# Kernel optimization log

Measured on AMD Instinct MI355X. Metric: run time of the kernel, lower is better.

## Reference

```python
import jax, jax.numpy as jnp
import numpy as np

N_NODES = 50000


def _gcn_layer(x, W, b, src, dst, n_nodes):
    # GCNConv: h = D^{-1/2} (A + I) D^{-1/2} (x W) + b, with src/dst already
    # including self-loops.
    h = x @ W  # [N, out]
    deg = jax.ops.segment_sum(jnp.ones(src.shape, x.dtype), dst,
                              num_segments=n_nodes)  # [N]
    dinv = jnp.where(deg > 0, jax.lax.rsqrt(jnp.maximum(deg, 1e-12)), 0.0)
    norm = dinv[src] * dinv[dst]  # [E+N]
    msg = h[src] * norm[:, None]  # gathered + weighted messages
    out = jax.ops.segment_sum(msg, dst, num_segments=n_nodes)  # scatter-add
    return out + b


def setup_inputs() -> dict:
    key = jax.random.key(0)
    k0, k1, k2, k3 = jax.random.split(key, 4)
    d_in, hidden, n_edges = 128, 128, 800000
    x = jax.random.normal(k0, (N_NODES, d_in), dtype=jnp.float32)
    edge_index = jax.random.randint(k1, (2, n_edges), 0, N_NODES, dtype=jnp.int64)
    W1 = jax.random.normal(k2, (d_in, hidden), dtype=jnp.float32) * (1.0 / np.sqrt(d_in))
    b1 = jnp.zeros((hidden,), jnp.float32)
    W2 = jax.random.normal(k3, (hidden, hidden), dtype=jnp.float32) * (1.0 / np.sqrt(hidden))
    b2 = jnp.zeros((hidden,), jnp.float32)
    return {"x": x, "edge_index": edge_index, "W1": W1, "b1": b1,
            "W2": W2, "b2": b2}


def reference(x, edge_index, W1, b1, W2, b2):
    n = x.shape[0]
    loop = jnp.arange(n, dtype=edge_index.dtype)
    src = jnp.concatenate([edge_index[0], loop])  # add self-loops
    dst = jnp.concatenate([edge_index[1], loop])
    h = _gcn_layer(x, W1, b1, src, dst, n)
    h = jax.nn.relu(h)
    # dropout p=0.5 is identity in eval mode (self.training == False)
    h = _gcn_layer(h, W2, b2, src, dst, n)
    return jax.nn.log_softmax(h, axis=1)
```

## Files before the change

kernel.cpp:

```cpp
#include <hip/hip_runtime.h>
#include <math.h>

#define D 128
#define CAP 6144
#define EPB 4096

typedef __attribute__((ext_vector_type(8))) short bf16x8;
typedef __attribute__((ext_vector_type(4))) float f32x4;

__device__ __forceinline__ float bf_lo(unsigned u) { return __uint_as_float(u << 16); }
__device__ __forceinline__ float bf_hi(unsigned u) { return __uint_as_float(u & 0xFFFF0000u); }
__device__ __forceinline__ unsigned pack_bf16(float a, float b) {
    unsigned ua = __float_as_uint(a), ub = __float_as_uint(b);
    ua = (ua + 0x7FFFu + ((ua >> 16) & 1u)) >> 16;
    ub = (ub + 0x7FFFu + ((ub >> 16) & 1u)) >> 16;
    return ua | (ub << 16);
}

__device__ __forceinline__ int edge_at(const void* eidx, int i64, long long pos) {
    return i64 ? (int)((const long long*)eidx)[pos] : ((const int*)eidx)[pos];
}


template <int AF32>
__device__ __forceinline__ void gemm_body(char* lds, int bid, const void* Ain,
                                          const float* __restrict__ Wf,
                                          const unsigned* __restrict__ metaIn,
                                          unsigned char* __restrict__ y8,
                                          float* __restrict__ scales, int n) {
    int tid = threadIdx.x;
    #pragma unroll
    for (int it = 0; it < 32; ++it) {
        int idx = tid + it * 256;
        int c = idx & 127, k2 = idx >> 7;
        *(unsigned*)&lds[c * 272 + k2 * 4] =
            pack_bf16(Wf[(k2 * 2) * D + c], Wf[(k2 * 2 + 1) * D + c]);
    }
    int w = tid >> 6, l = tid & 63;
    int row0 = bid * 128;
    int rowA0 = row0 + w * 16 + (l & 15);
    int rowA1 = rowA0 + 64;
    int rA0 = rowA0 < n ? rowA0 : 0;
    int rA1 = rowA1 < n ? rowA1 : 0;
    __syncthreads();

    f32x4 acc[2][8];
    #pragma unroll
    for (int r = 0; r < 2; ++r)
        #pragma unroll
        for (int f = 0; f < 8; ++f) acc[r][f] = (f32x4)0.f;

    #pragma unroll
    for (int s = 0; s < 4; ++s) {
        bf16x8 a0, a1;
        if (AF32) {
            const float* Af = (const float*)Ain;
            const float4* p0 = (const float4*)(Af + (size_t)rA0 * D + ((l >> 4) << 3) + s * 32);
            const float4* p1 = (const float4*)(Af + (size_t)rA1 * D + ((l >> 4) << 3) + s * 32);
            float4 f0 = p0[0], f1 = p0[1], f2 = p1[0], f3 = p1[1];
            uint4 v0, v1;
            v0.x = pack_bf16(f0.x, f0.y); v0.y = pack_bf16(f0.z, f0.w);
            v0.z = pack_bf16(f1.x, f1.y); v0.w = pack_bf16(f1.z, f1.w);
            v1.x = pack_bf16(f2.x, f2.y); v1.y = pack_bf16(f2.z, f2.w);
            v1.z = pack_bf16(f3.x, f3.y); v1.w = pack_bf16(f3.z, f3.w);
            a0 = *(bf16x8*)&v0;
            a1 = *(bf16x8*)&v1;
        } else {
            const char* Ab = (const char*)Ain;
            a0 = *(const bf16x8*)(Ab + (size_t)rA0 * 256 + ((l >> 4) << 4) + s * 64);
            a1 = *(const bf16x8*)(Ab + (size_t)rA1 * 256 + ((l >> 4) << 4) + s * 64);
        }
        int boff = ((l >> 4) << 4) + s * 64;
        #pragma unroll
        for (int f = 0; f < 8; ++f) {
            bf16x8 b = *(const bf16x8*)&lds[(f * 16 + (l & 15)) * 272 + boff];
            acc[0][f] = __builtin_amdgcn_mfma_f32_16x16x32_bf16(a0, b, acc[0][f], 0, 0, 0);
            acc[1][f] = __builtin_amdgcn_mfma_f32_16x16x32_bf16(a1, b, acc[1][f], 0, 0, 0);
        }
    }

    float* fl = (float*)lds;
    #pragma unroll
    for (int r = 0; r < 2; ++r) {
        __syncthreads();
        {
            int rbase = w * 16 + ((l >> 4) << 2);
            #pragma unroll
            for (int f = 0; f < 8; ++f) {
                int c = f * 16 + (l & 15);
                #pragma unroll
                for (int j = 0; j < 4; ++j)
                    fl[(rbase + j) * 132 + c] = acc[r][f][j];
            }
        }
        __syncthreads();
        int row = tid >> 2, cseg = (tid & 3) << 5;
        int gr = row0 + r * 64 + row;
        if (gr < n) {
            float z[32];
            #pragma unroll
            for (int i = 0; i < 32; ++i) z[i] = fl[row * 132 + cseg + i];
            float mx = 0.f;
            #pragma unroll
            for (int i = 0; i < 32; ++i) mx = fmaxf(mx, fabsf(z[i]));
            mx = fmaxf(mx, __shfl_xor(mx, 1));
            mx = fmaxf(mx, __shfl_xor(mx, 2));
            float inv = mx > 0.f ? 127.0f / mx : 0.f;
            unsigned q[8];
            #pragma unroll
            for (int j = 0; j < 8; ++j) {
                int q0 = __float2int_rn(z[j * 4 + 0] * inv);
                int q1 = __float2int_rn(z[j * 4 + 1] * inv);
                int q2 = __float2int_rn(z[j * 4 + 2] * inv);
                int q3 = __float2int_rn(z[j * 4 + 3] * inv);
                q[j] = (q0 & 255) | ((q1 & 255) << 8) | ((q2 & 255) << 16) | ((q3 & 255) << 24);
            }
            uint4* op = (uint4*)(y8 + (size_t)gr * 128 + cseg);
            op[0] = make_uint4(q[0], q[1], q[2], q[3]);
            op[1] = make_uint4(q[4], q[5], q[6], q[7]);
            if ((tid & 3) == 0) {
                float sc = mx * (1.0f / 127.0f);
                if (metaIn)
                    sc *= (float)(metaIn[gr] >> 17) * (1.0f / 32767.0f);
                scales[gr] = sc;
            }
        }
    }
}


__global__ void __launch_bounds__(256) k_prep(const void* eidx, int* bcnt,
                                              unsigned* __restrict__ binned, int e,
                                              const float* __restrict__ x,
                                              const float* __restrict__ W1,
                                              unsigned char* __restrict__ y8,
                                              float* __restrict__ scales,
                                              int n, int ebk) {
    __shared__ char lds[35840];
    int b = blockIdx.x, t = threadIdx.x;

    if (b >= ebk) {
        gemm_body<1>(lds, b - ebk, x, W1, nullptr, y8, scales, n);
        return;
    }

    int* hist = (int*)lds;
    int* gbase = hist + 256;
    int* lcur = gbase + 256;
    uint2* ed = (uint2*)(lds + 3072);

    const int* e32 = (const int*)eidx;
    int i64 = 1;
    #pragma unroll
    for (int j = 1; j < 32; j += 2)
        if (e32[j] != 0) i64 = 0;

    hist[t] = 0;
    lcur[t] = 0;
    __syncthreads();
    long long base = (long long)b * EPB;
    #pragma unroll
    for (int k = 0; k < EPB / 256; ++k) {
        long long i = base + k * 256 + t;
        if (i < e) {
            int s = edge_at(eidx, i64, i);
            int d = edge_at(eidx, i64, (long long)e + i);
            ed[k * 256 + t] = make_uint2((unsigned)s, (unsigned)d);
            atomicAdd(&hist[d >> 8], 1);
        }
    }
    __syncthreads();
    int c = hist[t];
    gbase[t] = c ? atomicAdd(&bcnt[t], c) : 0;
    __syncthreads();
    long long rem = e - base;
    int lim = (rem < EPB) ? (int)rem : EPB;
    for (int j = t; j < lim; j += 256) {
        uint2 sd = ed[j];
        int bk = sd.y >> 8;
        int off = gbase[bk] + atomicAdd(&lcur[bk], 1);
        if (off >= CAP) off = CAP - 1;
        binned[(size_t)bk * CAP + off] = sd.x | ((sd.y & 255u) << 17);
    }
}


__global__ void __launch_bounds__(256) k_binB(const unsigned* __restrict__ binned,
                                              const int* __restrict__ bcnt,
                                              const float* __restrict__ scales1,
                                              unsigned* __restrict__ meta,
                                              float* __restrict__ fs1,
                                              float* __restrict__ fs2,
                                              unsigned* __restrict__ csr64,
                                              int n) {
    __shared__ int lcur[256];
    int b = blockIdx.x, t = threadIdx.x;
    if (b == 0) {
        if (t == 0) meta[n] = 0;
        if (t == 1) fs1[n] = 0.f;
        if (t == 2) fs2[n] = 0.f;
    }
    lcur[t] = 0;
    __syncthreads();

    int cnt = bcnt[b];
    if (cnt > CAP) cnt = CAP;
    unsigned nodebase = (unsigned)b << 8;
    for (int i = t; i < cnt; i += 256) {
        unsigned en = binned[(size_t)b * CAP + i];
        unsigned src = en & 0x1FFFF;
        unsigned dl = en >> 17;
        int pos = atomicAdd(&lcur[dl], 1);
        if (pos < 64)
            csr64[(size_t)(nodebase + dl) * 64 + pos] = src;
    }
    __syncthreads();

    int node = b * 256 + t;
    if (node < n) {
        int dv = lcur[t];
        int filled = dv < 64 ? dv : 64;
        int pend = (filled + 7) & ~7;
        for (int j = filled; j < pend; ++j)
            csr64[(size_t)node * 64 + j] = (unsigned)n;
        unsigned q = __float2uint_rn(rsqrtf((float)(dv + 1)) * 32767.0f);
        meta[node] = (q << 17) | (unsigned)(pend >> 3);
        fs1[node] = ((float)q * (1.0f / 32767.0f)) * scales1[node];
    }
}


template <int EPI>
__global__ void __launch_bounds__(256) k_agg(const unsigned char* __restrict__ Y8,
                                             const float* __restrict__ fs,
                                             const unsigned* __restrict__ meta,
                                             const unsigned* __restrict__ csr64,
                                             const float* __restrict__ bias,
                                             void* __restrict__ outp, int n) {
    int node = __builtin_amdgcn_readfirstlane(blockIdx.x * 4 + (threadIdx.x >> 6));
    if (node >= n) return;
    int lane = threadIdx.x & 63;
    unsigned mt = meta[node];
    int pend = (mt & 15) << 3;
    float di = (float)(mt >> 17) * (1.0f / 32767.0f);
    const unsigned* cp = csr64 + (size_t)node * 64;
    const unsigned short* Yu = (const unsigned short*)Y8;

    unsigned su = Yu[(size_t)node * 64 + lane];
    float fself = fs[node];
    float ax = fself * (float)(char)(su & 255);
    float ay = fself * (float)(char)(su >> 8);

    for (int e = 0; e < pend; e += 8) {
        unsigned s0 = cp[e + 0], s1 = cp[e + 1], s2 = cp[e + 2], s3 = cp[e + 3];
        unsigned s4 = cp[e + 4], s5 = cp[e + 5], s6 = cp[e + 6], s7 = cp[e + 7];
        unsigned u0 = Yu[(size_t)s0 * 64 + lane];
        unsigned u1 = Yu[(size_t)s1 * 64 + lane];
        unsigned u2 = Yu[(size_t)s2 * 64 + lane];
        unsigned u3 = Yu[(size_t)s3 * 64 + lane];
        unsigned u4 = Yu[(size_t)s4 * 64 + lane];
        unsigned u5 = Yu[(size_t)s5 * 64 + lane];
        unsigned u6 = Yu[(size_t)s6 * 64 + lane];
        unsigned u7 = Yu[(size_t)s7 * 64 + lane];
        float f0 = fs[s0], f1 = fs[s1], f2 = fs[s2], f3 = fs[s3];
        float f4 = fs[s4], f5 = fs[s5], f6 = fs[s6], f7 = fs[s7];
        ax += f0 * (float)(char)(u0 & 255) + f1 * (float)(char)(u1 & 255)
            + f2 * (float)(char)(u2 & 255) + f3 * (float)(char)(u3 & 255)
            + f4 * (float)(char)(u4 & 255) + f5 * (float)(char)(u5 & 255)
            + f6 * (float)(char)(u6 & 255) + f7 * (float)(char)(u7 & 255);
        ay += f0 * (float)(char)(u0 >> 8) + f1 * (float)(char)(u1 >> 8)
            + f2 * (float)(char)(u2 >> 8) + f3 * (float)(char)(u3 >> 8)
            + f4 * (float)(char)(u4 >> 8) + f5 * (float)(char)(u5 >> 8)
            + f6 * (float)(char)(u6 >> 8) + f7 * (float)(char)(u7 >> 8);
    }

    float2 bv = ((const float2*)bias)[lane];
    float z0 = di * ax + bv.x;
    float z1 = di * ay + bv.y;

    if (EPI == 0) {
        ((unsigned*)outp)[(size_t)node * 64 + lane] =
            pack_bf16(fmaxf(z0, 0.f), fmaxf(z1, 0.f));
    } else {
        float m = fmaxf(z0, z1);
        #pragma unroll
        for (int off = 1; off < 64; off <<= 1) m = fmaxf(m, __shfl_xor(m, off));
        float s = __expf(z0 - m) + __expf(z1 - m);
        #pragma unroll
        for (int off = 1; off < 64; off <<= 1) s += __shfl_xor(s, off);
        float lse = m + __logf(s);
        ((float2*)outp)[(size_t)node * 64 + lane] = make_float2(z0 - lse, z1 - lse);
    }
}


__global__ void __launch_bounds__(256) k_gemm2(const unsigned* __restrict__ h,
                                               const float* __restrict__ W2,
                                               const unsigned* __restrict__ meta,
                                               unsigned char* __restrict__ y8b,
                                               float* __restrict__ fs2, int n) {
    __shared__ char lds[34816];
    gemm_body<0>(lds, blockIdx.x, h, W2, meta, y8b, fs2, n);
}


extern "C" void kernel_launch(void* const* d_in, const int* in_sizes, int n_in,
                              void* d_out, int out_size, void* d_ws, size_t ws_size,
                              hipStream_t stream) {
    const float* x  = (const float*)d_in[0];
    const void* eix = d_in[1];
    const float* W1 = (const float*)d_in[2];
    const float* b1 = (const float*)d_in[3];
    const float* W2 = (const float*)d_in[4];
    const float* b2 = (const float*)d_in[5];
    float* out = (float*)d_out;
    int n = in_sizes[0] / D;
    int e = in_sizes[1] / 2;

    char* p = (char*)d_ws;
    auto carve = [&](size_t bytes) -> void* {
        void* r = (void*)p;
        p += (bytes + 255) & ~(size_t)255;
        return r;
    };
    unsigned*      meta    = (unsigned*)carve((size_t)(n + 1) * 4);
    float*         fs1     = (float*)carve((size_t)(n + 1) * 4);
    float*         fs2     = (float*)carve((size_t)(n + 1) * 4);
    float*         scales1 = (float*)carve((size_t)(n + 1) * 4);
    int*           bcnt    = (int*)carve(1024);
    unsigned*      csr64   = (unsigned*)carve((size_t)n * 64 * 4);
    unsigned*      binned  = (unsigned*)carve((size_t)256 * CAP * 4);
    unsigned char* y8a     = (unsigned char*)carve((size_t)(n + 1) * 128);
    unsigned char* y8b     = (unsigned char*)carve((size_t)(n + 1) * 128);
    unsigned*      h       = (unsigned*)carve((size_t)n * 64 * 4);

    int nb = (n + 255) / 256;
    int ebk = (e + EPB - 1) / EPB;
    int gb = (n + 127) / 128;
    int ab = (n + 3) / 4;

    hipMemsetAsync(bcnt, 0, 1024, stream);
    k_prep<<<ebk + gb, 256, 0, stream>>>(eix, bcnt, binned, e, x, W1, y8a, scales1, n, ebk);
    k_binB<<<nb, 256, 0, stream>>>(binned, bcnt, scales1, meta, fs1, fs2, csr64, n);
    k_agg<0><<<ab, 256, 0, stream>>>(y8a, fs1, meta, csr64, b1, h, n);
    k_gemm2<<<gb, 256, 0, stream>>>(h, W2, meta, y8b, fs2, n);
    k_agg<1><<<ab, 256, 0, stream>>>(y8b, fs2, meta, csr64, b2, out, n);
}
```

Before: 117.5 us.

## Fuse layer-1 aggregation with layer-2 GEMM and quantization in one kernel

```diff
diff --git a/kernel.cpp b/kernel.cpp
--- a/kernel.cpp
+++ b/kernel.cpp
@@ -22,12 +22,10 @@
 }
 
 
-template <int AF32>
-__device__ __forceinline__ void gemm_body(char* lds, int bid, const void* Ain,
-                                          const float* __restrict__ Wf,
-                                          const unsigned* __restrict__ metaIn,
-                                          unsigned char* __restrict__ y8,
-                                          float* __restrict__ scales, int n) {
+__device__ __forceinline__ void gemm1_body(char* lds, int bid, const float* __restrict__ Af,
+                                           const float* __restrict__ Wf,
+                                           unsigned char* __restrict__ y8,
+                                           float* __restrict__ scales, int n) {
     int tid = threadIdx.x;
     #pragma unroll
     for (int it = 0; it < 32; ++it) {
@@ -52,24 +50,16 @@
 
     #pragma unroll
     for (int s = 0; s < 4; ++s) {
-        bf16x8 a0, a1;
-        if (AF32) {
-            const float* Af = (const float*)Ain;
-            const float4* p0 = (const float4*)(Af + (size_t)rA0 * D + ((l >> 4) << 3) + s * 32);
-            const float4* p1 = (const float4*)(Af + (size_t)rA1 * D + ((l >> 4) << 3) + s * 32);
-            float4 f0 = p0[0], f1 = p0[1], f2 = p1[0], f3 = p1[1];
-            uint4 v0, v1;
-            v0.x = pack_bf16(f0.x, f0.y); v0.y = pack_bf16(f0.z, f0.w);
-            v0.z = pack_bf16(f1.x, f1.y); v0.w = pack_bf16(f1.z, f1.w);
-            v1.x = pack_bf16(f2.x, f2.y); v1.y = pack_bf16(f2.z, f2.w);
-            v1.z = pack_bf16(f3.x, f3.y); v1.w = pack_bf16(f3.z, f3.w);
-            a0 = *(bf16x8*)&v0;
-            a1 = *(bf16x8*)&v1;
-        } else {
-            const char* Ab = (const char*)Ain;
-            a0 = *(const bf16x8*)(Ab + (size_t)rA0 * 256 + ((l >> 4) << 4) + s * 64);
-            a1 = *(const bf16x8*)(Ab + (size_t)rA1 * 256 + ((l >> 4) << 4) + s * 64);
-        }
+        const float4* p0 = (const float4*)(Af + (size_t)rA0 * D + ((l >> 4) << 3) + s * 32);
+        const float4* p1 = (const float4*)(Af + (size_t)rA1 * D + ((l >> 4) << 3) + s * 32);
+        float4 f0 = p0[0], f1 = p0[1], f2 = p1[0], f3 = p1[1];
+        uint4 v0, v1;
+        v0.x = pack_bf16(f0.x, f0.y); v0.y = pack_bf16(f0.z, f0.w);
+        v0.z = pack_bf16(f1.x, f1.y); v0.w = pack_bf16(f1.z, f1.w);
+        v1.x = pack_bf16(f2.x, f2.y); v1.y = pack_bf16(f2.z, f2.w);
+        v1.z = pack_bf16(f3.x, f3.y); v1.w = pack_bf16(f3.z, f3.w);
+        bf16x8 a0 = *(bf16x8*)&v0;
+        bf16x8 a1 = *(bf16x8*)&v1;
         int boff = ((l >> 4) << 4) + s * 64;
         #pragma unroll
         for (int f = 0; f < 8; ++f) {
@@ -118,12 +108,7 @@
             uint4* op = (uint4*)(y8 + (size_t)gr * 128 + cseg);
             op[0] = make_uint4(q[0], q[1], q[2], q[3]);
             op[1] = make_uint4(q[4], q[5], q[6], q[7]);
-            if ((tid & 3) == 0) {
-                float sc = mx * (1.0f / 127.0f);
-                if (metaIn)
-                    sc *= (float)(metaIn[gr] >> 17) * (1.0f / 32767.0f);
-                scales[gr] = sc;
-            }
+            if ((tid & 3) == 0) scales[gr] = mx * (1.0f / 127.0f);
         }
     }
 }
@@ -140,7 +125,7 @@
     int b = blockIdx.x, t = threadIdx.x;
 
     if (b >= ebk) {
-        gemm_body<1>(lds, b - ebk, x, W1, nullptr, y8, scales, n);
+        gemm1_body(lds, b - ebk, x, W1, y8, scales, n);
         return;
     }
 
@@ -230,13 +215,114 @@
 }
 
 
-template <int EPI>
-__global__ void __launch_bounds__(256) k_agg(const unsigned char* __restrict__ Y8,
-                                             const float* __restrict__ fs,
-                                             const unsigned* __restrict__ meta,
-                                             const unsigned* __restrict__ csr64,
-                                             const float* __restrict__ bias,
-                                             void* __restrict__ outp, int n) {
+__global__ void __launch_bounds__(1024) k_fuse(const unsigned char* __restrict__ Y8a,
+                                               const float* __restrict__ fs1,
+                                               const unsigned* __restrict__ meta,
+                                               const unsigned* __restrict__ csr64,
+                                               const float* __restrict__ b1,
+                                               const float* __restrict__ W2,
+                                               unsigned char* __restrict__ y8b,
+                                               float* __restrict__ fs2, int n) {
+    __shared__ char lds[39168];
+    char* Wld = lds;
+    char* Ald = lds + 34816;
+    int tid = threadIdx.x;
+
+    #pragma unroll
+    for (int it = 0; it < 8; ++it) {
+        int idx = tid + it * 1024;
+        int c = idx & 127, k2 = idx >> 7;
+        *(unsigned*)&Wld[c * 272 + k2 * 4] =
+            pack_bf16(W2[(k2 * 2) * D + c], W2[(k2 * 2 + 1) * D + c]);
+    }
+
+    int w = tid >> 6, l = tid & 63;
+    int node = blockIdx.x * 16 + w;
+
+    float z0 = 0.f, z1 = 0.f;
+    if (node < n) {
+        unsigned mt = meta[node];
+        int pend = (mt & 15) << 3;
+        float di = (float)(mt >> 17) * (1.0f / 32767.0f);
+        const unsigned* cp = csr64 + (size_t)node * 64;
+        const unsigned short* Yu = (const unsigned short*)Y8a;
+        unsigned su = Yu[(size_t)node * 64 + l];
+        float fself = fs1[node];
+        float ax = fself * (float)(char)(su & 255);
+        float ay = fself * (float)(char)(su >> 8);
+        for (int e2 = 0; e2 < pend; e2 += 8) {
+            unsigned s0 = cp[e2 + 0], s1 = cp[e2 + 1], s2 = cp[e2 + 2], s3 = cp[e2 + 3];
+            unsigned s4 = cp[e2 + 4], s5 = cp[e2 + 5], s6 = cp[e2 + 6], s7 = cp[e2 + 7];
+            unsigned u0 = Yu[(size_t)s0 * 64 + l];
+            unsigned u1 = Yu[(size_t)s1 * 64 + l];
+            unsigned u2 = Yu[(size_t)s2 * 64 + l];
+            unsigned u3 = Yu[(size_t)s3 * 64 + l];
+            unsigned u4 = Yu[(size_t)s4 * 64 + l];
+            unsigned u5 = Yu[(size_t)s5 * 64 + l];
+            unsigned u6 = Yu[(size_t)s6 * 64 + l];
+            unsigned u7 = Yu[(size_t)s7 * 64 + l];
+            float f0 = fs1[s0], f1 = fs1[s1], f2 = fs1[s2], f3 = fs1[s3];
+            float f4 = fs1[s4], f5 = fs1[s5], f6 = fs1[s6], f7 = fs1[s7];
+            ax += f0 * (float)(char)(u0 & 255) + f1 * (float)(char)(u1 & 255)
+                + f2 * (float)(char)(u2 & 255) + f3 * (float)(char)(u3 & 255)
+                + f4 * (float)(char)(u4 & 255) + f5 * (float)(char)(u5 & 255)
+                + f6 * (float)(char)(u6 & 255) + f7 * (float)(char)(u7 & 255);
+            ay += f0 * (float)(char)(u0 >> 8) + f1 * (float)(char)(u1 >> 8)
+                + f2 * (float)(char)(u2 >> 8) + f3 * (float)(char)(u3 >> 8)
+                + f4 * (float)(char)(u4 >> 8) + f5 * (float)(char)(u5 >> 8)
+                + f6 * (float)(char)(u6 >> 8) + f7 * (float)(char)(u7 >> 8);
+        }
+        float2 bv = ((const float2*)b1)[l];
+        z0 = fmaxf(di * ax + bv.x, 0.f);
+        z1 = fmaxf(di * ay + bv.y, 0.f);
+    }
+    *(unsigned*)&Ald[w * 272 + l * 4] = pack_bf16(z0, z1);
+    __syncthreads();
+
+    f32x4 acc = (f32x4)0.f;
+    if (w < 8) {
+        #pragma unroll
+        for (int s = 0; s < 4; ++s) {
+            int boff = ((l >> 4) << 4) + s * 64;
+            bf16x8 a = *(const bf16x8*)&Ald[(l & 15) * 272 + boff];
+            bf16x8 b = *(const bf16x8*)&Wld[(w * 16 + (l & 15)) * 272 + boff];
+            acc = __builtin_amdgcn_mfma_f32_16x16x32_bf16(a, b, acc, 0, 0, 0);
+        }
+    }
+    __syncthreads();
+
+    float* fl = (float*)lds;
+    if (w < 8) {
+        #pragma unroll
+        for (int j = 0; j < 4; ++j)
+            fl[(((l >> 4) << 2) + j) * 132 + w * 16 + (l & 15)] = acc[j];
+    }
+    __syncthreads();
+
+    if (node < n) {
+        float v0 = fl[w * 132 + l * 2];
+        float v1 = fl[w * 132 + l * 2 + 1];
+        float mx = fmaxf(fabsf(v0), fabsf(v1));
+        #pragma unroll
+        for (int off = 1; off < 64; off <<= 1) mx = fmaxf(mx, __shfl_xor(mx, off));
+        float inv = mx > 0.f ? 127.0f / mx : 0.f;
+        int q0 = __float2int_rn(v0 * inv);
+        int q1 = __float2int_rn(v1 * inv);
+        ((unsigned short*)y8b)[(size_t)node * 64 + l] =
+            (unsigned short)((q0 & 255) | ((q1 & 255) << 8));
+        if (l == 0)
+            fs2[node] = mx * (1.0f / 127.0f) *
+                        ((float)(meta[node] >> 17) * (1.0f / 32767.0f));
+    }
+}
+
+
+__global__ void __launch_bounds__(256) k_agg2(const unsigned char* __restrict__ Y8,
+                                              const float* __restrict__ fs,
+                                              const unsigned* __restrict__ meta,
+                                              const unsigned* __restrict__ csr64,
+                                              const float* __restrict__ bias,
+                                              float* __restrict__ outp, int n) {
     int node = __builtin_amdgcn_readfirstlane(blockIdx.x * 4 + (threadIdx.x >> 6));
     if (node >= n) return;
     int lane = threadIdx.x & 63;
@@ -278,29 +364,14 @@
     float z0 = di * ax + bv.x;
     float z1 = di * ay + bv.y;
 
-    if (EPI == 0) {
-        ((unsigned*)outp)[(size_t)node * 64 + lane] =
-            pack_bf16(fmaxf(z0, 0.f), fmaxf(z1, 0.f));
-    } else {
-        float m = fmaxf(z0, z1);
-        #pragma unroll
-        for (int off = 1; off < 64; off <<= 1) m = fmaxf(m, __shfl_xor(m, off));
-        float s = __expf(z0 - m) + __expf(z1 - m);
-        #pragma unroll
-        for (int off = 1; off < 64; off <<= 1) s += __shfl_xor(s, off);
-        float lse = m + __logf(s);
-        ((float2*)outp)[(size_t)node * 64 + lane] = make_float2(z0 - lse, z1 - lse);
-    }
-}
-
-
-__global__ void __launch_bounds__(256) k_gemm2(const unsigned* __restrict__ h,
-                                               const float* __restrict__ W2,
-                                               const unsigned* __restrict__ meta,
-                                               unsigned char* __restrict__ y8b,
-                                               float* __restrict__ fs2, int n) {
-    __shared__ char lds[34816];
-    gemm_body<0>(lds, blockIdx.x, h, W2, meta, y8b, fs2, n);
+    float m = fmaxf(z0, z1);
+    #pragma unroll
+    for (int off = 1; off < 64; off <<= 1) m = fmaxf(m, __shfl_xor(m, off));
+    float s = __expf(z0 - m) + __expf(z1 - m);
+    #pragma unroll
+    for (int off = 1; off < 64; off <<= 1) s += __shfl_xor(s, off);
+    float lse = m + __logf(s);
+    ((float2*)outp)[(size_t)node * 64 + lane] = make_float2(z0 - lse, z1 - lse);
 }
 
 
@@ -332,17 +403,16 @@
     unsigned*      binned  = (unsigned*)carve((size_t)256 * CAP * 4);
     unsigned char* y8a     = (unsigned char*)carve((size_t)(n + 1) * 128);
     unsigned char* y8b     = (unsigned char*)carve((size_t)(n + 1) * 128);
-    unsigned*      h       = (unsigned*)carve((size_t)n * 64 * 4);
 
     int nb = (n + 255) / 256;
     int ebk = (e + EPB - 1) / EPB;
     int gb = (n + 127) / 128;
+    int fb = (n + 15) / 16;
     int ab = (n + 3) / 4;
 
     hipMemsetAsync(bcnt, 0, 1024, stream);
     k_prep<<<ebk + gb, 256, 0, stream>>>(eix, bcnt, binned, e, x, W1, y8a, scales1, n, ebk);
     k_binB<<<nb, 256, 0, stream>>>(binned, bcnt, scales1, meta, fs1, fs2, csr64, n);
-    k_agg<0><<<ab, 256, 0, stream>>>(y8a, fs1, meta, csr64, b1, h, n);
-    k_gemm2<<<gb, 256, 0, stream>>>(h, W2, meta, y8b, fs2, n);
-    k_agg<1><<<ab, 256, 0, stream>>>(y8b, fs2, meta, csr64, b2, out, n);
-}
+    k_fuse<<<fb, 1024, 0, stream>>>(y8a, fs1, meta, csr64, b1, W2, y8b, fs2, n);
+    k_agg2<<<ab, 256, 0, stream>>>(y8b, fs2, meta, csr64, b2, out, n);
+}
```

Result: no change. 119.2 us (+1.4%).
